# Performance work log

Measured on AMD Instinct MI355X. Metric: run time of the kernel, lower is better.

Reference implementation:

```python
import jax, jax.numpy as jnp
import numpy as np

HEADS = 4
DIM_HEAD = 32
SCALE = DIM_HEAD ** -0.5


def setup_inputs() -> dict:
    key = jax.random.key(0)
    ks = jax.random.split(key, 7)
    b, c, h, w = 2, 256, 64, 64
    time_dim = 512
    hidden = HEADS * DIM_HEAD  # 128
    return {
        "x": jax.random.normal(ks[0], (b, c, h, w), jnp.float32),
        "time_emb": jax.random.normal(ks[1], (b, time_dim), jnp.float32),
        "w_mlp": jax.random.normal(ks[2], (2 * c, time_dim), jnp.float32) * 0.02,
        "b_mlp": jax.random.normal(ks[3], (2 * c,), jnp.float32) * 0.02,
        "w_qkv": jax.random.normal(ks[4], (3 * hidden, c), jnp.float32) * 0.05,
        "w_out": jax.random.normal(ks[5], (c, hidden), jnp.float32) * 0.05,
        "b_out": jax.random.normal(ks[6], (c,), jnp.float32) * 0.02,
    }


def reference(x, time_emb, w_mlp, b_mlp, w_qkv, w_out, b_out):
    b, c, h, w = x.shape
    n = h * w
    # FiLM conditioning: SiLU -> Linear -> chunk into (scale, shift)
    t = jax.nn.silu(time_emb) @ w_mlp.T + b_mlp            # [b, 2c]
    scale, shift = jnp.split(t, 2, axis=1)                  # [b, c] each
    x = x * (scale + 1.0)[:, :, None, None] + shift[:, :, None, None]
    # 1x1 conv QKV projection (no bias)
    qkv = jnp.einsum('oc,bchw->bohw', w_qkv, x)             # [b, 3*hidden, h, w]
    q, k, v = jnp.split(qkv, 3, axis=1)                     # [b, hidden, h, w]
    def to_heads(t):
        return t.reshape(b, HEADS, DIM_HEAD, n)             # b h d (x y)
    q, k, v = to_heads(q) * SCALE, to_heads(k), to_heads(v)
    sim = jnp.einsum('bhdi,bhdj->bhij', q, k)               # [b, h, n, n]
    attn = jax.nn.softmax(sim, axis=-1)
    out = jnp.einsum('bhij,bhdj->bhid', attn, v)            # [b, h, n, d]
    # b h (x y) d -> b (h d) x y
    out = out.transpose(0, 1, 3, 2).reshape(b, HEADS * DIM_HEAD, h, w)
    return jnp.einsum('oc,bchw->bohw', w_out, out) + b_out[None, :, None, None]
```

## Files before the change

kernel.cpp:

```cpp
#include <hip/hip_runtime.h>


typedef __bf16 bf16x8 __attribute__((ext_vector_type(8)));
typedef float  f32x16 __attribute__((ext_vector_type(16)));

#define MFMA(a, b, c) __builtin_amdgcn_mfma_f32_32x32x16_bf16((a), (b), (c), 0, 0, 0)

static constexpr float kLOG2E = 1.4426950408889634f;
static constexpr float kSCALE = 0.17677669529663687f;

__device__ __forceinline__ unsigned short bf16r(float x) {
  union { float f; unsigned u; } v; v.f = x;
  return (unsigned short)((v.u + 0x7FFFu + ((v.u >> 16) & 1u)) >> 16);
}
__device__ __forceinline__ float fast_silu(float x) {
  return x / (1.0f + __builtin_amdgcn_exp2f(-x * kLOG2E));
}
__device__ __forceinline__ f32x16 zero16() {
  f32x16 z;
#pragma unroll
  for (int i = 0; i < 16; ++i) z[i] = 0.0f;
  return z;
}
__device__ __forceinline__ bf16x8 ld_frag(const unsigned short* p) {
  return *reinterpret_cast<const bf16x8*>(p);
}

__global__ __launch_bounds__(64) void film1(const float* __restrict__ te,
                                            const float* __restrict__ w_mlp,
                                            const float* __restrict__ b_mlp,
                                            float* __restrict__ fparams) {
  int g = blockIdx.x * 64 + threadIdx.x;
  int pair = g >> 2, ks = g & 3;
  int b = pair >> 9, o = pair & 511;
  const float4* w4 = (const float4*)(w_mlp + (size_t)o * 512 + ks * 128);
  const float4* t4 = (const float4*)(te + (size_t)b * 512 + ks * 128);
  float s = 0.0f;
#pragma unroll 4
  for (int k = 0; k < 32; ++k) {
    float4 wv = w4[k];
    float4 tv = t4[k];
    s += wv.x * fast_silu(tv.x) + wv.y * fast_silu(tv.y) +
         wv.z * fast_silu(tv.z) + wv.w * fast_silu(tv.w);
  }
  s += __shfl_xor(s, 1, 64);
  s += __shfl_xor(s, 2, 64);
  if (ks == 0) {
    float t_val = s + b_mlp[o];
    fparams[b * 512 + o] = (o < 256) ? (t_val + 1.0f) : t_val;
  }
}

__global__ __launch_bounds__(64) void film2(const float* __restrict__ w_qkv,
                                            const float* __restrict__ fparams,
                                            const float* __restrict__ w_out,
                                            unsigned short* __restrict__ Aeff,
                                            float* __restrict__ qb,
                                            unsigned short* __restrict__ WoBf) {
  int tid = blockIdx.x * 64 + threadIdx.x;
  if (tid < 1536) {
    int row = tid >> 1, cs = tid & 1;
    int b = row / 384, o = row % 384;
    float qs = (o < 128) ? (kSCALE * kLOG2E) : 1.0f;
    const float4* wr  = (const float4*)(w_qkv + (size_t)o * 256);
    const float4* sc4 = (const float4*)(fparams + b * 512);
    const float4* sh4 = (const float4*)(fparams + b * 512 + 256);
    unsigned short* arow = Aeff + ((size_t)b * 384 + o) * 256;
    float acc = 0.0f;
#pragma unroll 4
    for (int i = 0; i < 32; ++i) {
      int c4 = cs * 32 + i;
      float4 wv = wr[c4], scv = sc4[c4], shv = sh4[c4];
      acc += wv.x * shv.x + wv.y * shv.y + wv.z * shv.z + wv.w * shv.w;
      union { unsigned short u[4]; unsigned long long q; } pk;
      pk.u[0] = bf16r(wv.x * scv.x * qs);
      pk.u[1] = bf16r(wv.y * scv.y * qs);
      pk.u[2] = bf16r(wv.z * scv.z * qs);
      pk.u[3] = bf16r(wv.w * scv.w * qs);
      *(unsigned long long*)(arow + c4 * 4) = pk.q;
    }
    acc += __shfl_xor(acc, 1, 64);
    if (cs == 0) qb[b * 384 + o] = acc * qs;
  } else {
    int t = tid - 1536;
    const float4* src = (const float4*)(w_out + (size_t)t * 64);
    unsigned short* dst = WoBf + (size_t)t * 64;
#pragma unroll 4
    for (int i = 0; i < 16; ++i) {
      float4 v = src[i];
      union { unsigned short u[4]; unsigned long long q; } pk;
      pk.u[0] = bf16r(v.x); pk.u[1] = bf16r(v.y);
      pk.u[2] = bf16r(v.z); pk.u[3] = bf16r(v.w);
      *(unsigned long long*)(dst + i * 4) = pk.q;
    }
  }
}

__global__ __launch_bounds__(256) void xpose(const float* __restrict__ x,
                                             unsigned short* __restrict__ xT) {
  __shared__ unsigned short lds[64][66];
  int bid = blockIdx.x;
  int p0 = (bid & 63) * 64;
  int c0 = ((bid >> 6) & 3) * 64;
  int b  = bid >> 8;
  int t = threadIdx.x;
  int pl = t & 63, cw = t >> 6;
  const float* xb = x + ((size_t)b * 256 + c0) * 4096 + p0;
#pragma unroll
  for (int r = 0; r < 16; ++r) {
    int cl = cw + r * 4;
    lds[pl][cl] = bf16r(xb[(size_t)cl * 4096 + pl]);
  }
  __syncthreads();
  unsigned short* out = xT + ((size_t)b * 4096 + p0) * 256 + c0;
#pragma unroll
  for (int rep = 0; rep < 2; ++rep) {
    int ch = t + rep * 256;
    int pr = ch >> 3, cc = (ch & 7) * 8;
    union { unsigned short u[8]; uint4 v; } pk;
#pragma unroll
    for (int i = 0; i < 8; ++i) pk.u[i] = lds[pr][cc + i];
    *(uint4*)(out + (size_t)pr * 256 + cc) = pk.v;
  }
}

__global__ __launch_bounds__(64) void qkv_gemm(const unsigned short* __restrict__ Aeff,
                                               const float* __restrict__ qb,
                                               const unsigned short* __restrict__ xT,
                                               unsigned short* __restrict__ Qb,
                                               unsigned short* __restrict__ Kb,
                                               unsigned short* __restrict__ Vt) {
  int bid = blockIdx.x;
  int o_blk = bid % 12;
  int rest = bid / 12;
  int b = rest & 1, p_blk = rest >> 1;
  int l = threadIdx.x, col = l & 31, hi = l >> 5;

  const unsigned short* Ab = Aeff + ((size_t)b * 384 + o_blk * 32) * 256;
  const unsigned short* Bb = xT + ((size_t)b * 4096 + p_blk * 32) * 256;

  f32x16 acc = zero16();
#pragma unroll
  for (int kc = 0; kc < 256; kc += 16) {
    bf16x8 a0 = ld_frag(Ab + (size_t)col * 256 + kc + hi * 8);
    bf16x8 b0 = ld_frag(Bb + (size_t)col * 256 + kc + hi * 8);
    acc = MFMA(a0, b0, acc);
  }

  int obase = o_blk * 32;
  int sec = obase >> 7;
  int head = (obase & 127) >> 5;
  size_t bh = (size_t)b * 4 + head;
  int p = p_blk * 32 + col;
  if (sec < 2) {
    unsigned short* dst = (sec == 0 ? Qb : Kb) + (bh * 4096 + p) * 32;
#pragma unroll
    for (int g = 0; g < 4; ++g) {
      int dbase = 8 * g + 4 * hi;
      union { unsigned short u[4]; unsigned long long q; } pk;
#pragma unroll
      for (int r = 0; r < 4; ++r)
        pk.u[r] = bf16r(acc[4 * g + r] + qb[b * 384 + obase + dbase + r]);
      *(unsigned long long*)(dst + dbase) = pk.q;
    }
  } else {
    unsigned short* dst = Vt + bh * 32 * 4096;
#pragma unroll
    for (int reg = 0; reg < 16; ++reg) {
      int d = (reg & 3) + 8 * (reg >> 2) + 4 * hi;
      dst[(size_t)d * 4096 + p] = bf16r(acc[reg] + qb[b * 384 + obase + d]);
    }
  }
}

__global__ __launch_bounds__(256) void attn(const unsigned short* __restrict__ Qb,
                                            const unsigned short* __restrict__ Kb,
                                            const unsigned short* __restrict__ Vt,
                                            unsigned short* __restrict__ Ob) {
  __shared__ float Olds[4][16][64];
  __shared__ float mlds[4][64];
  __shared__ float llds[4][64];

  int bid = blockIdx.x;
  int bh = bid >> 7;
  int q0 = (bid & 127) * 32;
  int w = threadIdx.x >> 6;
  int l = threadIdx.x & 63, col = l & 31, hi = l >> 5;

  const unsigned short* Qp = Qb + ((size_t)bh * 4096 + q0) * 32;
  const unsigned short* Kp = Kb + (size_t)bh * 4096 * 32;
  const unsigned short* Vp = Vt + (size_t)bh * 32 * 4096;

  bf16x8 qf0 = ld_frag(Qp + col * 32 + hi * 8);
  bf16x8 qf1 = ld_frag(Qp + col * 32 + 16 + hi * 8);

  f32x16 O = zero16();
  float m = -1e30f, lsum = 0.0f;

  for (int kt = w * 32; kt < w * 32 + 32; ++kt) {
    const unsigned short* krow = Kp + ((size_t)kt * 32 + col) * 32 + hi * 8;
    bf16x8 ka0 = ld_frag(krow);
    bf16x8 ka1 = ld_frag(krow + 16);
    const unsigned short* vrow = Vp + (size_t)col * 4096 + kt * 32 + hi * 8;
    bf16x8 va0 = ld_frag(vrow);
    bf16x8 va1 = ld_frag(vrow + 16);

    f32x16 S = MFMA(ka0, qf0, zero16());
    S = MFMA(ka1, qf1, S);

    float t0 = fmaxf(S[0], S[1]),  t1 = fmaxf(S[2], S[3]);
    float t2 = fmaxf(S[4], S[5]),  t3 = fmaxf(S[6], S[7]);
    float t4 = fmaxf(S[8], S[9]),  t5 = fmaxf(S[10], S[11]);
    float t6 = fmaxf(S[12], S[13]), t7 = fmaxf(S[14], S[15]);
    float pmax = fmaxf(fmaxf(fmaxf(t0, t1), fmaxf(t2, t3)),
                       fmaxf(fmaxf(t4, t5), fmaxf(t6, t7)));
    pmax = fmaxf(pmax, __shfl_xor(pmax, 32, 64));

    if (!__all(pmax <= m + 8.0f)) {
      float mnew = fmaxf(m, pmax);
      float r = __builtin_amdgcn_exp2f(m - mnew);
      lsum *= r;
#pragma unroll
      for (int i = 0; i < 16; ++i) O[i] *= r;
      m = mnew;
    }

    float P[16];
#pragma unroll
    for (int i = 0; i < 16; ++i) P[i] = __builtin_amdgcn_exp2f(S[i] - m);
    float s0 = (P[0] + P[1]) + (P[2] + P[3]);
    float s1 = (P[4] + P[5]) + (P[6] + P[7]);
    float s2 = (P[8] + P[9]) + (P[10] + P[11]);
    float s3 = (P[12] + P[13]) + (P[14] + P[15]);
    lsum += (s0 + s1) + (s2 + s3);

    union { __bf16 h[16]; unsigned u[8]; } pu;
#pragma unroll
    for (int i = 0; i < 16; ++i) pu.h[i] = (__bf16)P[i];
    unsigned pp[8];
#pragma unroll
    for (int j = 0; j < 8; ++j) pp[j] = (unsigned)__shfl_xor((int)pu.u[j], 32, 64);

    union { unsigned u[4]; bf16x8 v; } B0, B1;
    if (hi == 0) {
      B0.u[0] = pu.u[0]; B0.u[1] = pu.u[1]; B0.u[2] = pp[0]; B0.u[3] = pp[1];
      B1.u[0] = pu.u[4]; B1.u[1] = pu.u[5]; B1.u[2] = pp[4]; B1.u[3] = pp[5];
    } else {
      B0.u[0] = pp[2]; B0.u[1] = pp[3]; B0.u[2] = pu.u[2]; B0.u[3] = pu.u[3];
      B1.u[0] = pp[6]; B1.u[1] = pp[7]; B1.u[2] = pu.u[6]; B1.u[3] = pu.u[7];
    }
    O = MFMA(va0, B0.v, O);
    O = MFMA(va1, B1.v, O);
  }

  float lt = lsum + __shfl_xor(lsum, 32, 64);

#pragma unroll
  for (int i = 0; i < 16; ++i) Olds[w][i][l] = O[i];
  mlds[w][l] = m;
  llds[w][l] = lt;
  __syncthreads();

  float m0 = mlds[0][l], m1 = mlds[1][l], m2 = mlds[2][l], m3 = mlds[3][l];
  float M = fmaxf(fmaxf(m0, m1), fmaxf(m2, m3));
  float w0 = __builtin_amdgcn_exp2f(m0 - M);
  float w1 = __builtin_amdgcn_exp2f(m1 - M);
  float w2 = __builtin_amdgcn_exp2f(m2 - M);
  float w3 = __builtin_amdgcn_exp2f(m3 - M);
  float L = llds[0][l] * w0 + llds[1][l] * w1 + llds[2][l] * w2 + llds[3][l] * w3;
  float inv = 1.0f / L;

  unsigned short* dst = Ob + ((size_t)bh * 4096 + q0 + col) * 32 + 8 * w + 4 * hi;
  union { unsigned short u[4]; unsigned long long q; } pkout;
#pragma unroll
  for (int r = 0; r < 4; ++r) {
    int reg = 4 * w + r;
    float val = Olds[0][reg][l] * w0 + Olds[1][reg][l] * w1 +
                Olds[2][reg][l] * w2 + Olds[3][reg][l] * w3;
    pkout.u[r] = bf16r(val * inv);
  }
  *(unsigned long long*)dst = pkout.q;
}

__global__ __launch_bounds__(64) void out_gemm(const unsigned short* __restrict__ Wo,
                                               const unsigned short* __restrict__ Ob,
                                               const float* __restrict__ b_out,
                                               float* __restrict__ out) {
  int bid = blockIdx.x;
  int o_blk = bid & 7;
  int rest = bid >> 3;
  int b = rest & 1, p_blk = rest >> 1;
  int l = threadIdx.x, col = l & 31, hi = l >> 5;

  const unsigned short* Ab = Wo + (size_t)(o_blk * 32) * 128;
  f32x16 acc = zero16();
#pragma unroll
  for (int kc = 0; kc < 128; kc += 16) {
    int head = kc >> 5;
    int doff = (kc & 16) + hi * 8;
    const unsigned short* Bb =
        Ob + (((size_t)b * 4 + head) * 4096 + p_blk * 32) * 32 + doff;
    bf16x8 a0 = ld_frag(Ab + (size_t)col * 128 + kc + hi * 8);
    bf16x8 b0 = ld_frag(Bb + (size_t)col * 32);
    acc = MFMA(a0, b0, acc);
  }
  int p = p_blk * 32 + col;
#pragma unroll
  for (int reg = 0; reg < 16; ++reg) {
    int o = o_blk * 32 + (reg & 3) + 8 * (reg >> 2) + 4 * hi;
    out[((size_t)b * 256 + o) * 4096 + p] = acc[reg] + b_out[o];
  }
}

extern "C" void kernel_launch(void* const* d_in, const int* in_sizes, int n_in,
                              void* d_out, int out_size, void* d_ws, size_t ws_size,
                              hipStream_t stream) {
  const float* x     = (const float*)d_in[0];
  const float* te    = (const float*)d_in[1];
  const float* w_mlp = (const float*)d_in[2];
  const float* b_mlp = (const float*)d_in[3];
  const float* w_qkv = (const float*)d_in[4];
  const float* w_out = (const float*)d_in[5];
  const float* b_out = (const float*)d_in[6];

  char* ws = (char*)d_ws;
  float*          fparams = (float*)(ws + 0);
  float*          qb      = (float*)(ws + 4096);
  unsigned short* Aeff    = (unsigned short*)(ws + 8192);
  unsigned short* WoBf    = (unsigned short*)(ws + 401408);
  unsigned short* xT      = (unsigned short*)(ws + 466944);
  unsigned short* Qb      = (unsigned short*)(ws + 4661248);
  unsigned short* Kb      = (unsigned short*)(ws + 6758400);
  unsigned short* Vt      = (unsigned short*)(ws + 8855552);
  unsigned short* Ob      = (unsigned short*)(ws + 10952704);
  float* out = (float*)d_out;

  hipLaunchKernelGGL(film1, dim3(64), dim3(64), 0, stream, te, w_mlp, b_mlp, fparams);
  hipLaunchKernelGGL(film2, dim3(32), dim3(64), 0, stream, w_qkv, fparams, w_out,
                     Aeff, qb, WoBf);
  hipLaunchKernelGGL(xpose, dim3(512), dim3(256), 0, stream, x, xT);
  hipLaunchKernelGGL(qkv_gemm, dim3(3072), dim3(64), 0, stream, Aeff, qb, xT, Qb, Kb, Vt);
  hipLaunchKernelGGL(attn, dim3(1024), dim3(256), 0, stream, Qb, Kb, Vt, Ob);
  hipLaunchKernelGGL(out_gemm, dim3(2048), dim3(64), 0, stream, WoBf, Ob, b_out, out);
}
```

Baseline: 156.1 us.

## Merge FiLM and transpose kernels, widen attention split-K, use permlane32 swaps

```diff
diff --git a/kernel.cpp b/kernel.cpp
--- a/kernel.cpp
+++ b/kernel.cpp
@@ -3,8 +3,10 @@
 
 typedef __bf16 bf16x8 __attribute__((ext_vector_type(8)));
 typedef float  f32x16 __attribute__((ext_vector_type(16)));
+typedef unsigned uint2v __attribute__((ext_vector_type(2)));
 
 #define MFMA(a, b, c) __builtin_amdgcn_mfma_f32_32x32x16_bf16((a), (b), (c), 0, 0, 0)
+#define PLSWAP(a, b) __builtin_amdgcn_permlane32_swap((a), (b), false, false)
 
 static constexpr float kLOG2E = 1.4426950408889634f;
 static constexpr float kSCALE = 0.17677669529663687f;
@@ -26,40 +28,71 @@
   return *reinterpret_cast<const bf16x8*>(p);
 }
 
-__global__ __launch_bounds__(64) void film1(const float* __restrict__ te,
+__global__ __launch_bounds__(256) void prep(const float* __restrict__ x,
+                                            unsigned short* __restrict__ xT,
+                                            const float* __restrict__ te,
                                             const float* __restrict__ w_mlp,
                                             const float* __restrict__ b_mlp,
                                             float* __restrict__ fparams) {
-  int g = blockIdx.x * 64 + threadIdx.x;
-  int pair = g >> 2, ks = g & 3;
-  int b = pair >> 9, o = pair & 511;
-  const float4* w4 = (const float4*)(w_mlp + (size_t)o * 512 + ks * 128);
-  const float4* t4 = (const float4*)(te + (size_t)b * 512 + ks * 128);
-  float s = 0.0f;
+  __shared__ unsigned short lds[64][66];
+  int bid = blockIdx.x;
+  if (bid < 32) {
+    int g = bid * 256 + threadIdx.x;
+    int pair = g >> 3, ks = g & 7;
+    int b = pair >> 9, o = pair & 511;
+    const float4* w4 = (const float4*)(w_mlp + (size_t)o * 512 + ks * 64);
+    const float4* t4 = (const float4*)(te + (size_t)b * 512 + ks * 64);
+    float s = 0.0f;
 #pragma unroll 4
-  for (int k = 0; k < 32; ++k) {
-    float4 wv = w4[k];
-    float4 tv = t4[k];
-    s += wv.x * fast_silu(tv.x) + wv.y * fast_silu(tv.y) +
-         wv.z * fast_silu(tv.z) + wv.w * fast_silu(tv.w);
-  }
-  s += __shfl_xor(s, 1, 64);
-  s += __shfl_xor(s, 2, 64);
-  if (ks == 0) {
-    float t_val = s + b_mlp[o];
-    fparams[b * 512 + o] = (o < 256) ? (t_val + 1.0f) : t_val;
-  }
-}
-
-__global__ __launch_bounds__(64) void film2(const float* __restrict__ w_qkv,
-                                            const float* __restrict__ fparams,
-                                            const float* __restrict__ w_out,
-                                            unsigned short* __restrict__ Aeff,
-                                            float* __restrict__ qb,
-                                            unsigned short* __restrict__ WoBf) {
-  int tid = blockIdx.x * 64 + threadIdx.x;
-  if (tid < 1536) {
-    int row = tid >> 1, cs = tid & 1;
+    for (int k = 0; k < 16; ++k) {
+      float4 wv = w4[k];
+      float4 tv = t4[k];
+      s += wv.x * fast_silu(tv.x) + wv.y * fast_silu(tv.y) +
+           wv.z * fast_silu(tv.z) + wv.w * fast_silu(tv.w);
+    }
+    s += __shfl_xor(s, 1, 64);
+    s += __shfl_xor(s, 2, 64);
+    s += __shfl_xor(s, 4, 64);
+    if (ks == 0) {
+      float t_val = s + b_mlp[o];
+      fparams[b * 512 + o] = (o < 256) ? (t_val + 1.0f) : t_val;
+    }
+    return;
+  }
+  int bid2 = bid - 32;
+  int p0 = (bid2 & 63) * 64;
+  int c0 = ((bid2 >> 6) & 3) * 64;
+  int b  = bid2 >> 8;
+  int t = threadIdx.x;
+  int pl = t & 63, cw = t >> 6;
+  const float* xb = x + ((size_t)b * 256 + c0) * 4096 + p0;
+#pragma unroll
+  for (int r = 0; r < 16; ++r) {
+    int cl = cw + r * 4;
+    lds[pl][cl] = bf16r(xb[(size_t)cl * 4096 + pl]);
+  }
+  __syncthreads();
+  unsigned short* out = xT + ((size_t)b * 4096 + p0) * 256 + c0;
+#pragma unroll
+  for (int rep = 0; rep < 2; ++rep) {
+    int ch = t + rep * 256;
+    int pr = ch >> 3, cc = (ch & 7) * 8;
+    union { unsigned short u[8]; uint4 v; } pk;
+#pragma unroll
+    for (int i = 0; i < 8; ++i) pk.u[i] = lds[pr][cc + i];
+    *(uint4*)(out + (size_t)pr * 256 + cc) = pk.v;
+  }
+}
+
+__global__ __launch_bounds__(256) void film2(const float* __restrict__ w_qkv,
+                                             const float* __restrict__ fparams,
+                                             const float* __restrict__ w_out,
+                                             unsigned short* __restrict__ Aeff,
+                                             float* __restrict__ qb,
+                                             unsigned short* __restrict__ WoBf) {
+  int tid = blockIdx.x * 256 + threadIdx.x;
+  if (tid < 3072) {
+    int row = tid >> 2, cs = tid & 3;
     int b = row / 384, o = row % 384;
     float qs = (o < 128) ? (kSCALE * kLOG2E) : 1.0f;
     const float4* wr  = (const float4*)(w_qkv + (size_t)o * 256);
@@ -68,8 +101,8 @@
     unsigned short* arow = Aeff + ((size_t)b * 384 + o) * 256;
     float acc = 0.0f;
 #pragma unroll 4
-    for (int i = 0; i < 32; ++i) {
-      int c4 = cs * 32 + i;
+    for (int i = 0; i < 16; ++i) {
+      int c4 = cs * 16 + i;
       float4 wv = wr[c4], scv = sc4[c4], shv = sh4[c4];
       acc += wv.x * shv.x + wv.y * shv.y + wv.z * shv.z + wv.w * shv.w;
       union { unsigned short u[4]; unsigned long long q; } pk;
@@ -80,9 +113,10 @@
       *(unsigned long long*)(arow + c4 * 4) = pk.q;
     }
     acc += __shfl_xor(acc, 1, 64);
+    acc += __shfl_xor(acc, 2, 64);
     if (cs == 0) qb[b * 384 + o] = acc * qs;
   } else {
-    int t = tid - 1536;
+    int t = tid - 3072;
     const float4* src = (const float4*)(w_out + (size_t)t * 64);
     unsigned short* dst = WoBf + (size_t)t * 64;
 #pragma unroll 4
@@ -93,34 +127,6 @@
       pk.u[2] = bf16r(v.z); pk.u[3] = bf16r(v.w);
       *(unsigned long long*)(dst + i * 4) = pk.q;
     }
-  }
-}
-
-__global__ __launch_bounds__(256) void xpose(const float* __restrict__ x,
-                                             unsigned short* __restrict__ xT) {
-  __shared__ unsigned short lds[64][66];
-  int bid = blockIdx.x;
-  int p0 = (bid & 63) * 64;
-  int c0 = ((bid >> 6) & 3) * 64;
-  int b  = bid >> 8;
-  int t = threadIdx.x;
-  int pl = t & 63, cw = t >> 6;
-  const float* xb = x + ((size_t)b * 256 + c0) * 4096 + p0;
-#pragma unroll
-  for (int r = 0; r < 16; ++r) {
-    int cl = cw + r * 4;
-    lds[pl][cl] = bf16r(xb[(size_t)cl * 4096 + pl]);
-  }
-  __syncthreads();
-  unsigned short* out = xT + ((size_t)b * 4096 + p0) * 256 + c0;
-#pragma unroll
-  for (int rep = 0; rep < 2; ++rep) {
-    int ch = t + rep * 256;
-    int pr = ch >> 3, cc = (ch & 7) * 8;
-    union { unsigned short u[8]; uint4 v; } pk;
-#pragma unroll
-    for (int i = 0; i < 8; ++i) pk.u[i] = lds[pr][cc + i];
-    *(uint4*)(out + (size_t)pr * 256 + cc) = pk.v;
   }
 }
 
@@ -173,13 +179,13 @@
   }
 }
 
-__global__ __launch_bounds__(256) void attn(const unsigned short* __restrict__ Qb,
+__global__ __launch_bounds__(512) void attn(const unsigned short* __restrict__ Qb,
                                             const unsigned short* __restrict__ Kb,
                                             const unsigned short* __restrict__ Vt,
                                             unsigned short* __restrict__ Ob) {
-  __shared__ float Olds[4][16][64];
-  __shared__ float mlds[4][64];
-  __shared__ float llds[4][64];
+  __shared__ float Olds[8][16][64];
+  __shared__ float mlds[8][64];
+  __shared__ float llds[8][64];
 
   int bid = blockIdx.x;
   int bh = bid >> 7;
@@ -188,25 +194,27 @@
   int l = threadIdx.x & 63, col = l & 31, hi = l >> 5;
 
   const unsigned short* Qp = Qb + ((size_t)bh * 4096 + q0) * 32;
-  const unsigned short* Kp = Kb + (size_t)bh * 4096 * 32;
-  const unsigned short* Vp = Vt + (size_t)bh * 32 * 4096;
 
   bf16x8 qf0 = ld_frag(Qp + col * 32 + hi * 8);
   bf16x8 qf1 = ld_frag(Qp + col * 32 + 16 + hi * 8);
 
+  const unsigned short* kp =
+      Kb + (size_t)bh * 4096 * 32 + ((size_t)(w * 16) * 32 + col) * 32 + hi * 8;
+  const unsigned short* vp =
+      Vt + (size_t)bh * 32 * 4096 + (size_t)col * 4096 + (w * 16) * 32 + hi * 8;
+
   f32x16 O = zero16();
   float m = -1e30f, lsum = 0.0f;
 
-  for (int kt = w * 32; kt < w * 32 + 32; ++kt) {
-    const unsigned short* krow = Kp + ((size_t)kt * 32 + col) * 32 + hi * 8;
-    bf16x8 ka0 = ld_frag(krow);
-    bf16x8 ka1 = ld_frag(krow + 16);
-    const unsigned short* vrow = Vp + (size_t)col * 4096 + kt * 32 + hi * 8;
-    bf16x8 va0 = ld_frag(vrow);
-    bf16x8 va1 = ld_frag(vrow + 16);
+  for (int it = 0; it < 16; ++it, kp += 1024, vp += 32) {
+    bf16x8 ka0 = ld_frag(kp);
+    bf16x8 ka1 = ld_frag(kp + 16);
 
     f32x16 S = MFMA(ka0, qf0, zero16());
     S = MFMA(ka1, qf1, S);
+
+    bf16x8 va0 = ld_frag(vp);
+    bf16x8 va1 = ld_frag(vp + 16);
 
     float t0 = fmaxf(S[0], S[1]),  t1 = fmaxf(S[2], S[3]);
     float t2 = fmaxf(S[4], S[5]),  t3 = fmaxf(S[6], S[7]);
@@ -214,7 +222,8 @@
     float t6 = fmaxf(S[12], S[13]), t7 = fmaxf(S[14], S[15]);
     float pmax = fmaxf(fmaxf(fmaxf(t0, t1), fmaxf(t2, t3)),
                        fmaxf(fmaxf(t4, t5), fmaxf(t6, t7)));
-    pmax = fmaxf(pmax, __shfl_xor(pmax, 32, 64));
+    uint2v mm = PLSWAP(__float_as_uint(pmax), __float_as_uint(pmax));
+    pmax = fmaxf(__uint_as_float(mm[0]), __uint_as_float(mm[1]));
 
     if (!__all(pmax <= m + 8.0f)) {
       float mnew = fmaxf(m, pmax);
@@ -225,35 +234,31 @@
       m = mnew;
     }
 
-    float P[16];
-#pragma unroll
-    for (int i = 0; i < 16; ++i) P[i] = __builtin_amdgcn_exp2f(S[i] - m);
-    float s0 = (P[0] + P[1]) + (P[2] + P[3]);
-    float s1 = (P[4] + P[5]) + (P[6] + P[7]);
-    float s2 = (P[8] + P[9]) + (P[10] + P[11]);
-    float s3 = (P[12] + P[13]) + (P[14] + P[15]);
+#pragma unroll
+    for (int i = 0; i < 16; ++i) S[i] = __builtin_amdgcn_exp2f(S[i] - m);
+    float s0 = (S[0] + S[1]) + (S[2] + S[3]);
+    float s1 = (S[4] + S[5]) + (S[6] + S[7]);
+    float s2 = (S[8] + S[9]) + (S[10] + S[11]);
+    float s3 = (S[12] + S[13]) + (S[14] + S[15]);
     lsum += (s0 + s1) + (s2 + s3);
 
     union { __bf16 h[16]; unsigned u[8]; } pu;
 #pragma unroll
-    for (int i = 0; i < 16; ++i) pu.h[i] = (__bf16)P[i];
-    unsigned pp[8];
-#pragma unroll
-    for (int j = 0; j < 8; ++j) pp[j] = (unsigned)__shfl_xor((int)pu.u[j], 32, 64);
-
+    for (int i = 0; i < 16; ++i) pu.h[i] = (__bf16)S[i];
+    uint2v r0 = PLSWAP(pu.u[0], pu.u[2]);
+    uint2v r1 = PLSWAP(pu.u[1], pu.u[3]);
+    uint2v r2 = PLSWAP(pu.u[4], pu.u[6]);
+    uint2v r3 = PLSWAP(pu.u[5], pu.u[7]);
     union { unsigned u[4]; bf16x8 v; } B0, B1;
-    if (hi == 0) {
-      B0.u[0] = pu.u[0]; B0.u[1] = pu.u[1]; B0.u[2] = pp[0]; B0.u[3] = pp[1];
-      B1.u[0] = pu.u[4]; B1.u[1] = pu.u[5]; B1.u[2] = pp[4]; B1.u[3] = pp[5];
-    } else {
-      B0.u[0] = pp[2]; B0.u[1] = pp[3]; B0.u[2] = pu.u[2]; B0.u[3] = pu.u[3];
-      B1.u[0] = pp[6]; B1.u[1] = pp[7]; B1.u[2] = pu.u[6]; B1.u[3] = pu.u[7];
-    }
+    B0.u[0] = r0[0]; B0.u[1] = r1[0]; B0.u[2] = r0[1]; B0.u[3] = r1[1];
+    B1.u[0] = r2[0]; B1.u[1] = r3[0]; B1.u[2] = r2[1]; B1.u[3] = r3[1];
+
     O = MFMA(va0, B0.v, O);
     O = MFMA(va1, B1.v, O);
   }
 
-  float lt = lsum + __shfl_xor(lsum, 32, 64);
+  uint2v lr = PLSWAP(__float_as_uint(lsum), __float_as_uint(lsum));
+  float lt = __uint_as_float(lr[0]) + __uint_as_float(lr[1]);
 
 #pragma unroll
   for (int i = 0; i < 16; ++i) Olds[w][i][l] = O[i];
@@ -261,25 +266,32 @@
   llds[w][l] = lt;
   __syncthreads();
 
-  float m0 = mlds[0][l], m1 = mlds[1][l], m2 = mlds[2][l], m3 = mlds[3][l];
-  float M = fmaxf(fmaxf(m0, m1), fmaxf(m2, m3));
-  float w0 = __builtin_amdgcn_exp2f(m0 - M);
-  float w1 = __builtin_amdgcn_exp2f(m1 - M);
-  float w2 = __builtin_amdgcn_exp2f(m2 - M);
-  float w3 = __builtin_amdgcn_exp2f(m3 - M);
-  float L = llds[0][l] * w0 + llds[1][l] * w1 + llds[2][l] * w2 + llds[3][l] * w3;
+  float mv[8];
+  float M = -1e30f;
+#pragma unroll
+  for (int i = 0; i < 8; ++i) { mv[i] = mlds[i][l]; M = fmaxf(M, mv[i]); }
+  float wgt[8];
+  float L = 0.0f;
+#pragma unroll
+  for (int i = 0; i < 8; ++i) {
+    wgt[i] = __builtin_amdgcn_exp2f(mv[i] - M);
+    L += llds[i][l] * wgt[i];
+  }
   float inv = 1.0f / L;
 
-  unsigned short* dst = Ob + ((size_t)bh * 4096 + q0 + col) * 32 + 8 * w + 4 * hi;
-  union { unsigned short u[4]; unsigned long long q; } pkout;
-#pragma unroll
-  for (int r = 0; r < 4; ++r) {
-    int reg = 4 * w + r;
-    float val = Olds[0][reg][l] * w0 + Olds[1][reg][l] * w1 +
-                Olds[2][reg][l] * w2 + Olds[3][reg][l] * w3;
-    pkout.u[r] = bf16r(val * inv);
-  }
-  *(unsigned long long*)dst = pkout.q;
+  int reg0 = 2 * w;
+  float v0 = 0.0f, v1 = 0.0f;
+#pragma unroll
+  for (int i = 0; i < 8; ++i) {
+    v0 += Olds[i][reg0][l] * wgt[i];
+    v1 += Olds[i][reg0 + 1][l] * wgt[i];
+  }
+  int based = 8 * (w >> 1) + 2 * (w & 1) + 4 * hi;
+  unsigned short* dst = Ob + ((size_t)bh * 4096 + q0 + col) * 32 + based;
+  union { unsigned short u[2]; unsigned q; } pk2;
+  pk2.u[0] = bf16r(v0 * inv);
+  pk2.u[1] = bf16r(v1 * inv);
+  *(unsigned*)dst = pk2.q;
 }
 
 __global__ __launch_bounds__(64) void out_gemm(const unsigned short* __restrict__ Wo,
@@ -335,11 +347,11 @@
   unsigned short* Ob      = (unsigned short*)(ws + 10952704);
   float* out = (float*)d_out;
 
-  hipLaunchKernelGGL(film1, dim3(64), dim3(64), 0, stream, te, w_mlp, b_mlp, fparams);
-  hipLaunchKernelGGL(film2, dim3(32), dim3(64), 0, stream, w_qkv, fparams, w_out,
+  hipLaunchKernelGGL(prep, dim3(544), dim3(256), 0, stream, x, xT, te, w_mlp,
+                     b_mlp, fparams);
+  hipLaunchKernelGGL(film2, dim3(14), dim3(256), 0, stream, w_qkv, fparams, w_out,
                      Aeff, qb, WoBf);
-  hipLaunchKernelGGL(xpose, dim3(512), dim3(256), 0, stream, x, xT);
   hipLaunchKernelGGL(qkv_gemm, dim3(3072), dim3(64), 0, stream, Aeff, qb, xT, Qb, Kb, Vt);
-  hipLaunchKernelGGL(attn, dim3(1024), dim3(256), 0, stream, Qb, Kb, Vt, Ob);
+  hipLaunchKernelGGL(attn, dim3(1024), dim3(512), 0, stream, Qb, Kb, Vt, Ob);
   hipLaunchKernelGGL(out_gemm, dim3(2048), dim3(64), 0, stream, WoBf, Ob, b_out, out);
 }
```

Result: no change. 153.8 us (-1.5%).
